# Performance work log

Measured on AMD Instinct MI355X. Metric: run time of the kernel, lower is better.

## Reference

```python
import jax, jax.numpy as jnp
import numpy as np

EPS = 1e-12  # torch spectral_norm default eps


def _l2norm(v):
    return v / (jnp.linalg.norm(v) + EPS)


def _spectral_norm_2d(w, u):
    # one power iteration (torch default n_power_iterations=1), u/v detached
    v = _l2norm(w.T @ u)
    u_new = _l2norm(w @ v)
    u_new = jax.lax.stop_gradient(u_new)
    v = jax.lax.stop_gradient(v)
    sigma = u_new @ (w @ v)
    return w / sigma


def _spectral_norm_1d(b):
    # torch._SpectralNorm for ndim==1: F.normalize(weight, dim=0)
    return b / (jnp.linalg.norm(b) + EPS)


def setup_inputs() -> dict:
    key = jax.random.key(0)
    ks = jax.random.split(key, 8)
    T, B, I, H = 4096, 32, 256, 256
    s_i = 1.0 / np.sqrt(H)  # nn.RNN init: U(-1/sqrt(H), 1/sqrt(H))
    return {
        "x": jax.random.normal(ks[0], (T, B, I), jnp.float32),
        "state": jax.random.normal(ks[1], (1, B, H), jnp.float32),
        "w_ih": jax.random.uniform(ks[2], (H, I), jnp.float32, -s_i, s_i),
        "w_hh": jax.random.uniform(ks[3], (H, H), jnp.float32, -s_i, s_i),
        "b_ih": jax.random.uniform(ks[4], (H,), jnp.float32, -s_i, s_i),
        "b_hh": jax.random.uniform(ks[5], (H,), jnp.float32, -s_i, s_i),
        "u_ih": jax.random.normal(ks[6], (H,), jnp.float32),  # power-iteration buffer
        "u_hh": jax.random.normal(ks[7], (H,), jnp.float32),
    }


def reference(x, state, w_ih, w_hh, b_ih, b_hh, u_ih, u_hh):
    # spectral-norm parametrization of all RNN weights
    w_ih_sn = _spectral_norm_2d(w_ih, _l2norm(u_ih))
    w_hh_sn = _spectral_norm_2d(w_hh, _l2norm(u_hh))
    b_sn = _spectral_norm_1d(b_ih) + _spectral_norm_1d(b_hh)

    # input projection batched over all timesteps: [T,B,H]
    pre = jnp.einsum("tbi,hi->tbh", x, w_ih_sn) + b_sn

    def step(h, p):
        h_new = jnp.tanh(p + h @ w_hh_sn.T)
        return h_new, h_new

    h_last, out = jax.lax.scan(step, state[0], pre)
    return out, h_last[None]
```

## Files before the change

kernel.cpp:

```cpp
#include <hip/hip_runtime.h>
#include <hip/hip_bf16.h>
#include <math.h>

#define EPSF 1e-12f
#define H 256
#define TSTEPS 4096
#define BATCH 32
#define TB (TSTEPS*BATCH)
#define BH (BATCH*H)

typedef _Float16 h2 __attribute__((ext_vector_type(2)));

#if defined(__has_builtin)
#if __has_builtin(__builtin_amdgcn_fdot2)
#define FDOT2(a, b, c) __builtin_amdgcn_fdot2((a), (b), (c), false)
#endif
#endif
#ifndef FDOT2
#define FDOT2(a, b, c) fmaf((float)(a).y, (float)(b).y, fmaf((float)(a).x, (float)(b).x, (c)))
#endif

#define BC(u) __builtin_bit_cast(h2, (u))

#define DPPF(x, ctrl) __builtin_bit_cast(float, __builtin_amdgcn_update_dpp( \
    0, __builtin_bit_cast(int, (x)), (ctrl), 0xf, 0xf, true))
#define DPP_QUAD_XOR1 0xB1
#define DPP_QUAD_XOR2 0x4E
#define DPP_HALF_MIRROR 0x141
#define DPP_ROW_MIRROR  0x140

__device__ __forceinline__ void bar_nodrain() {
  __builtin_amdgcn_sched_barrier(0);
  asm volatile("s_waitcnt lgkmcnt(0)" ::: "memory");
  __builtin_amdgcn_s_barrier();
  __builtin_amdgcn_sched_barrier(0);
}

__device__ __forceinline__ float block_sum256(float v, float* red) {
  #pragma unroll
  for (int o = 32; o > 0; o >>= 1) v += __shfl_down(v, o, 64);
  __syncthreads();
  if ((threadIdx.x & 63) == 0) red[threadIdx.x >> 6] = v;
  __syncthreads();
  return red[0] + red[1] + red[2] + red[3];
}

__global__ __launch_bounds__(256) void k_prep(
    const float* __restrict__ w_ih, const float* __restrict__ w_hh,
    const float* __restrict__ b_ih, const float* __restrict__ b_hh,
    const float* __restrict__ u_ih, const float* __restrict__ u_hh,
    float* __restrict__ wsc) {
  __shared__ float red[4];
  __shared__ float ubuf[H];
  __shared__ float vbuf[H];
  const int tid = threadIdx.x;

  float inv_sig[2];
  const float* Ws[2] = {w_ih, w_hh};
  const float* Us[2] = {u_ih, u_hh};
  #pragma unroll 1
  for (int m = 0; m < 2; m++) {
    const float* W = Ws[m];
    float uv = Us[m][tid];
    float nu = sqrtf(block_sum256(uv * uv, red));
    ubuf[tid] = uv / (nu + EPSF);
    __syncthreads();
    float vt = 0.f;
    for (int h = 0; h < H; h++) vt = fmaf(W[h * H + tid], ubuf[h], vt);
    float nv = sqrtf(block_sum256(vt * vt, red));
    vbuf[tid] = vt / (nv + EPSF);
    __syncthreads();
    float wv = 0.f;
    const float* wr = W + (size_t)tid * H;
    for (int i = 0; i < H; i++) wv = fmaf(wr[i], vbuf[i], wv);
    float n2 = block_sum256(wv * wv, red);
    float sigma = n2 / (sqrtf(n2) + EPSF);
    inv_sig[m] = 1.f / sigma;
  }
  float bi = b_ih[tid], bh = b_hh[tid];
  float nbi = sqrtf(block_sum256(bi * bi, red));
  float nbh = sqrtf(block_sum256(bh * bh, red));
  wsc[tid] = bi / (nbi + EPSF) + bh / (nbh + EPSF);
  if (tid == 0) { wsc[H] = inv_sig[0]; wsc[H + 1] = inv_sig[1]; }
}

__global__ __launch_bounds__(256) void k_pre(
    const float* __restrict__ x, const float* __restrict__ w_ih,
    const float* __restrict__ wsc, float* __restrict__ pre) {
  __shared__ float xs[64 * 256];
  const int tid = threadIdx.x;
  const size_t m0 = (size_t)blockIdx.x * 64;

  const float4* xp = (const float4*)(x + m0 * H);
  float4* xsv = (float4*)xs;
  #pragma unroll
  for (int j = 0; j < 16; j++) xsv[j * 256 + tid] = xp[j * 256 + tid];
  __syncthreads();

  const int hg = tid & 31;
  const int mg = tid >> 5;
  const int h0 = hg << 3;
  const int mr0 = mg << 3;

  float acc[8][8];
  #pragma unroll
  for (int i = 0; i < 8; i++)
    #pragma unroll
    for (int j = 0; j < 8; j++) acc[i][j] = 0.f;

  const float* wbase = w_ih + (size_t)h0 * H;
  #pragma unroll 1
  for (int kb = 0; kb < 256; kb += 4) {
    float4 w[8];
    #pragma unroll
    for (int j = 0; j < 8; j++)
      w[j] = *(const float4*)(wbase + (size_t)j * H + kb);
    #pragma unroll
    for (int i = 0; i < 8; i++) {
      float4 xv = *(const float4*)(xs + (mr0 + i) * 256 + kb);
      #pragma unroll
      for (int j = 0; j < 8; j++) {
        float a = acc[i][j];
        a = fmaf(xv.x, w[j].x, a);
        a = fmaf(xv.y, w[j].y, a);
        a = fmaf(xv.z, w[j].z, a);
        a = fmaf(xv.w, w[j].w, a);
        acc[i][j] = a;
      }
    }
  }
  const float inv_s = wsc[H];
  float bs[8];
  #pragma unroll
  for (int j = 0; j < 8; j++) bs[j] = wsc[h0 + j];
  #pragma unroll
  for (int i = 0; i < 8; i++) {
    float4 o0, o1;
    o0.x = fmaf(acc[i][0], inv_s, bs[0]);
    o0.y = fmaf(acc[i][1], inv_s, bs[1]);
    o0.z = fmaf(acc[i][2], inv_s, bs[2]);
    o0.w = fmaf(acc[i][3], inv_s, bs[3]);
    o1.x = fmaf(acc[i][4], inv_s, bs[4]);
    o1.y = fmaf(acc[i][5], inv_s, bs[5]);
    o1.z = fmaf(acc[i][6], inv_s, bs[6]);
    o1.w = fmaf(acc[i][7], inv_s, bs[7]);
    float* pr = pre + (m0 + mr0 + i) * H + h0;
    *(float4*)pr = o0;
    *(float4*)(pr + 4) = o1;
  }
}

__device__ __forceinline__ int swz(int a) { return a ^ (((a >> 8) & 1) << 6); }

__global__ __launch_bounds__(512, 1) void k_scan(
    const float* __restrict__ state, const float* __restrict__ w_hh,
    const float* __restrict__ wsc, float* __restrict__ out) {
  __shared__ __align__(16) _Float16 hbuf[2][H];
  const int tid = threadIdx.x;
  const int cg   = tid >> 6;
  const int q    = tid & 63;
  const int rgrp = q >> 4;
  const int kseg = q & 15;
  const int jrow = 4 * ((q >> 3) & 1) + 2 * ((q >> 2) & 1) + ((q >> 1) & 1);
  const int myrow = (cg << 5) + (rgrp << 3) + jrow;
  const int b = blockIdx.x;
  const float inv_s = wsc[H + 1];
  const bool hb3 = (q >> 3) & 1, hb2 = (q >> 2) & 1, hb1 = (q >> 1) & 1;

  h2 wreg[8][8];
  #pragma unroll
  for (int i = 0; i < 8; i++) {
    const float* wr = w_hh + (size_t)((cg << 5) + (rgrp << 3) + i) * H + (kseg << 4);
    #pragma unroll
    for (int c = 0; c < 8; c++) {
      float2 wv = *(const float2*)(wr + 2 * c);
      wreg[i][c] = h2{(_Float16)(wv.x * inv_s), (_Float16)(wv.y * inv_s)};
    }
  }

  const int a0s = swz(kseg << 5);
  const int a1s = swz((kseg << 5) + 16);
  const int woff = swz(myrow * 2);

  if (tid < H)
    *(_Float16*)((char*)&hbuf[0][0] + swz(tid * 2)) = (_Float16)state[b * H + tid];

  const float* pbase = out + (size_t)b * H + myrow;
  float pre0 = pbase[0], pre1 = pbase[BH];
  bar_nodrain();

  float hn = 0.f;
  #pragma unroll 1
  for (int t = 0; t < TSTEPS; t++) {
    int tn = (t + 2 <= TSTEPS) ? (t + 2) : TSTEPS;
    float pre2 = pbase[(size_t)tn * BH];

    const char* hb = (const char*)&hbuf[t & 1][0];
    uint4 q0 = *(const uint4*)(hb + a0s);
    uint4 q1 = *(const uint4*)(hb + a1s);

    float acc[8];
    #pragma unroll
    for (int i = 0; i < 8; i++) {
      float a = 0.f;
      a = FDOT2(wreg[i][0], BC(q0.x), a);
      a = FDOT2(wreg[i][1], BC(q0.y), a);
      a = FDOT2(wreg[i][2], BC(q0.z), a);
      a = FDOT2(wreg[i][3], BC(q0.w), a);
      a = FDOT2(wreg[i][4], BC(q1.x), a);
      a = FDOT2(wreg[i][5], BC(q1.y), a);
      a = FDOT2(wreg[i][6], BC(q1.z), a);
      a = FDOT2(wreg[i][7], BC(q1.w), a);
      acc[i] = a;
    }

    float v0, v1, v2, v3;
    { float k0 = hb3 ? acc[4] : acc[0], s0 = hb3 ? acc[0] : acc[4];
      float k1 = hb3 ? acc[5] : acc[1], s1 = hb3 ? acc[1] : acc[5];
      float k2 = hb3 ? acc[6] : acc[2], s2 = hb3 ? acc[2] : acc[6];
      float k3 = hb3 ? acc[7] : acc[3], s3 = hb3 ? acc[3] : acc[7];
      v0 = k0 + DPPF(s0, DPP_ROW_MIRROR);
      v1 = k1 + DPPF(s1, DPP_ROW_MIRROR);
      v2 = k2 + DPPF(s2, DPP_ROW_MIRROR);
      v3 = k3 + DPPF(s3, DPP_ROW_MIRROR); }
    float u0, u1;
    { float k0 = hb2 ? v2 : v0, s0 = hb2 ? v0 : v2;
      float k1 = hb2 ? v3 : v1, s1 = hb2 ? v1 : v3;
      u0 = k0 + DPPF(s0, DPP_HALF_MIRROR);
      u1 = k1 + DPPF(s1, DPP_HALF_MIRROR); }
    float ssum;
    { float k0 = hb1 ? u1 : u0, s0 = hb1 ? u0 : u1;
      ssum = k0 + DPPF(s0, DPP_QUAD_XOR2); }
    ssum += DPPF(ssum, DPP_QUAD_XOR1);

    float s = ssum + pre0;
    float sc = fminf(fmaxf(s, -15.f), 15.f);
    float e = __expf(2.f * sc);
    hn = __fdividef(e - 1.f, e + 1.f);

    if (!(q & 1)) {
      *(_Float16*)((char*)&hbuf[(t + 1) & 1][0] + woff) = (_Float16)hn;
      out[(size_t)t * BH + b * H + myrow] = hn;
    }
    bar_nodrain();
    pre0 = pre1; pre1 = pre2;
  }
  if (!(q & 1)) out[(size_t)TSTEPS * BH + b * H + myrow] = hn;
}

extern "C" void kernel_launch(void* const* d_in, const int* in_sizes, int n_in,
                              void* d_out, int out_size, void* d_ws, size_t ws_size,
                              hipStream_t stream) {
  const float* x     = (const float*)d_in[0];
  const float* state = (const float*)d_in[1];
  const float* w_ih  = (const float*)d_in[2];
  const float* w_hh  = (const float*)d_in[3];
  const float* b_ih  = (const float*)d_in[4];
  const float* b_hh  = (const float*)d_in[5];
  const float* u_ih  = (const float*)d_in[6];
  const float* u_hh  = (const float*)d_in[7];
  float* out = (float*)d_out;
  float* wsc = (float*)d_ws;

  k_prep<<<1, 256, 0, stream>>>(w_ih, w_hh, b_ih, b_hh, u_ih, u_hh, wsc);
  k_pre<<<TB / 64, 256, 0, stream>>>(x, w_ih, wsc, out);
  k_scan<<<BATCH, 512, 0, stream>>>(state, w_hh, wsc, out);
}
```

Baseline: 2.882 ms.

## Pre-scale and transpose w_ih to fp16; use packed fp16 FMA in scan dot products

Adds a kernel that scales w_ih by its spectral-norm inverse and stores it transposed in fp16, so the projection GEMM reads half the weight bytes with contiguous per-k rows and skips the final scale multiply. The recurrent scan replaces the chain of fdot2 fp32-accumulate ops with packed fp16 multiply-adds, followed by one fdot2 reduction into fp32, which shortens the serial per-step instruction chain. Both changes lower precision: fp16 weights in the input projection, and fp16 accumulation inside the recurrence, which could let error build up over 4096 steps.

```diff
diff --git a/kernel.cpp b/kernel.cpp
--- a/kernel.cpp
+++ b/kernel.cpp
@@ -84,8 +84,15 @@
   if (tid == 0) { wsc[H] = inv_sig[0]; wsc[H + 1] = inv_sig[1]; }
 }
 
+__global__ __launch_bounds__(256) void k_wcvt(
+    const float* __restrict__ w_ih, const float* __restrict__ wsc,
+    _Float16* __restrict__ wt) {
+  const int h = blockIdx.x, k = threadIdx.x;
+  wt[(size_t)k * H + h] = (_Float16)(w_ih[(size_t)h * H + k] * wsc[H]);
+}
+
 __global__ __launch_bounds__(256) void k_pre(
-    const float* __restrict__ x, const float* __restrict__ w_ih,
+    const float* __restrict__ x, const _Float16* __restrict__ wt,
     const float* __restrict__ wsc, float* __restrict__ pre) {
   __shared__ float xs[64 * 256];
   const int tid = threadIdx.x;
@@ -108,42 +115,46 @@
     #pragma unroll
     for (int j = 0; j < 8; j++) acc[i][j] = 0.f;
 
-  const float* wbase = w_ih + (size_t)h0 * H;
   #pragma unroll 1
   for (int kb = 0; kb < 256; kb += 4) {
-    float4 w[8];
-    #pragma unroll
-    for (int j = 0; j < 8; j++)
-      w[j] = *(const float4*)(wbase + (size_t)j * H + kb);
+    float wf[4][8];
+    #pragma unroll
+    for (int j = 0; j < 4; j++) {
+      uint4 wv = *(const uint4*)(wt + (size_t)(kb + j) * H + h0);
+      h2 p0 = BC(wv.x), p1 = BC(wv.y), p2 = BC(wv.z), p3 = BC(wv.w);
+      wf[j][0] = (float)p0.x; wf[j][1] = (float)p0.y;
+      wf[j][2] = (float)p1.x; wf[j][3] = (float)p1.y;
+      wf[j][4] = (float)p2.x; wf[j][5] = (float)p2.y;
+      wf[j][6] = (float)p3.x; wf[j][7] = (float)p3.y;
+    }
     #pragma unroll
     for (int i = 0; i < 8; i++) {
       float4 xv = *(const float4*)(xs + (mr0 + i) * 256 + kb);
       #pragma unroll
       for (int j = 0; j < 8; j++) {
         float a = acc[i][j];
-        a = fmaf(xv.x, w[j].x, a);
-        a = fmaf(xv.y, w[j].y, a);
-        a = fmaf(xv.z, w[j].z, a);
-        a = fmaf(xv.w, w[j].w, a);
+        a = fmaf(xv.x, wf[0][j], a);
+        a = fmaf(xv.y, wf[1][j], a);
+        a = fmaf(xv.z, wf[2][j], a);
+        a = fmaf(xv.w, wf[3][j], a);
         acc[i][j] = a;
       }
     }
   }
-  const float inv_s = wsc[H];
   float bs[8];
   #pragma unroll
   for (int j = 0; j < 8; j++) bs[j] = wsc[h0 + j];
   #pragma unroll
   for (int i = 0; i < 8; i++) {
     float4 o0, o1;
-    o0.x = fmaf(acc[i][0], inv_s, bs[0]);
-    o0.y = fmaf(acc[i][1], inv_s, bs[1]);
-    o0.z = fmaf(acc[i][2], inv_s, bs[2]);
-    o0.w = fmaf(acc[i][3], inv_s, bs[3]);
-    o1.x = fmaf(acc[i][4], inv_s, bs[4]);
-    o1.y = fmaf(acc[i][5], inv_s, bs[5]);
-    o1.z = fmaf(acc[i][6], inv_s, bs[6]);
-    o1.w = fmaf(acc[i][7], inv_s, bs[7]);
+    o0.x = acc[i][0] + bs[0];
+    o0.y = acc[i][1] + bs[1];
+    o0.z = acc[i][2] + bs[2];
+    o0.w = acc[i][3] + bs[3];
+    o1.x = acc[i][4] + bs[4];
+    o1.y = acc[i][5] + bs[5];
+    o1.z = acc[i][6] + bs[6];
+    o1.w = acc[i][7] + bs[7];
     float* pr = pre + (m0 + mr0 + i) * H + h0;
     *(float4*)pr = o0;
     *(float4*)(pr + 4) = o1;
@@ -166,6 +177,7 @@
   const int b = blockIdx.x;
   const float inv_s = wsc[H + 1];
   const bool hb3 = (q >> 3) & 1, hb2 = (q >> 2) & 1, hb1 = (q >> 1) & 1;
+  const h2 one2 = h2{(_Float16)1.f, (_Float16)1.f};
 
   h2 wreg[8][8];
   #pragma unroll
@@ -202,16 +214,15 @@
     float acc[8];
     #pragma unroll
     for (int i = 0; i < 8; i++) {
-      float a = 0.f;
-      a = FDOT2(wreg[i][0], BC(q0.x), a);
-      a = FDOT2(wreg[i][1], BC(q0.y), a);
-      a = FDOT2(wreg[i][2], BC(q0.z), a);
-      a = FDOT2(wreg[i][3], BC(q0.w), a);
-      a = FDOT2(wreg[i][4], BC(q1.x), a);
-      a = FDOT2(wreg[i][5], BC(q1.y), a);
-      a = FDOT2(wreg[i][6], BC(q1.z), a);
-      a = FDOT2(wreg[i][7], BC(q1.w), a);
-      acc[i] = a;
+      h2 a2 = wreg[i][0] * BC(q0.x);
+      a2 = wreg[i][1] * BC(q0.y) + a2;
+      a2 = wreg[i][2] * BC(q0.z) + a2;
+      a2 = wreg[i][3] * BC(q0.w) + a2;
+      a2 = wreg[i][4] * BC(q1.x) + a2;
+      a2 = wreg[i][5] * BC(q1.y) + a2;
+      a2 = wreg[i][6] * BC(q1.z) + a2;
+      a2 = wreg[i][7] * BC(q1.w) + a2;
+      acc[i] = FDOT2(a2, one2, 0.f);
     }
 
     float v0, v1, v2, v3;
@@ -261,8 +272,10 @@
   const float* u_hh  = (const float*)d_in[7];
   float* out = (float*)d_out;
   float* wsc = (float*)d_ws;
+  _Float16* wt = (_Float16*)((char*)d_ws + 2048);
 
   k_prep<<<1, 256, 0, stream>>>(w_ih, w_hh, b_ih, b_hh, u_ih, u_hh, wsc);
-  k_pre<<<TB / 64, 256, 0, stream>>>(x, w_ih, wsc, out);
+  k_wcvt<<<H, 256, 0, stream>>>(w_ih, wsc, wt);
+  k_pre<<<TB / 64, 256, 0, stream>>>(x, wt, wsc, out);
   k_scan<<<BATCH, 512, 0, stream>>>(state, w_hh, wsc, out);
 }
```

Result: no change. 2.909 ms (+0.9%).
